# Kernel optimization log

Measured on AMD Instinct MI355X. Metric: run time of the kernel, lower is better.

## Reference

```python
import jax, jax.numpy as jnp
import numpy as np

B, N, NPOINT, K = 8, 8192, 1024, 32
MLP = [64, 64, 128]
EPS = 1e-5  # torch BatchNorm2d default eps


def setup_inputs() -> dict:
    key = jax.random.key(0)
    ks = jax.random.split(key, 1 + 2 * len(MLP))
    inp = {"xyz": jax.random.normal(ks[0], (B, N, 3), jnp.float32)}
    last = 3
    for i, o in enumerate(MLP):
        inp[f"w{i}"] = jax.random.normal(ks[1 + 2 * i], (o, last), jnp.float32) / np.float32(np.sqrt(last))
        inp[f"b{i}"] = jax.random.normal(ks[2 + 2 * i], (o,), jnp.float32) * 0.01
        inp[f"g{i}"] = jnp.ones((o,), jnp.float32)   # BN weight
        inp[f"be{i}"] = jnp.zeros((o,), jnp.float32)  # BN bias
        last = o
    return inp


def farthest_point_sample(xyz, npoint):
    # Sequential FPS; deterministic start at index 0 (original torch uses randint).
    Bb, Nn, _ = xyz.shape

    def step(carry, _):
        distance, farthest = carry
        centroid = jnp.take_along_axis(xyz, farthest[:, None, None], axis=1)  # [B,1,3]
        dist = jnp.sum((xyz - centroid) ** 2, -1)                              # [B,N]
        distance = jnp.minimum(distance, dist)
        nxt = jnp.argmax(distance, -1)
        return (distance, nxt), farthest

    init = (jnp.full((Bb, Nn), 1e10, xyz.dtype), jnp.zeros((Bb,), jnp.int32))
    _, cents = jax.lax.scan(step, init, None, length=npoint)
    return cents.T  # [B, npoint]


def _forward(xyz, params):
    fps_idx = farthest_point_sample(xyz, NPOINT)
    fps_idx = jax.lax.stop_gradient(fps_idx)
    new_xyz = jnp.take_along_axis(xyz, fps_idx[:, :, None], axis=1)  # [B,npoint,3]
    # squared pairwise distances [B, npoint, N]
    d = (jnp.sum(new_xyz ** 2, -1)[:, :, None]
         + jnp.sum(xyz ** 2, -1)[:, None, :]
         - 2.0 * jnp.einsum('bmc,bnc->bmn', new_xyz, xyz))
    _, idx = jax.lax.top_k(-d, K)  # k nearest neighbors, [B,npoint,k]
    grouped = jax.vmap(lambda pts, i: pts[i])(xyz, idx)  # [B,npoint,k,3]
    feat = grouped - new_xyz[:, :, None, :]              # grouped_xyz_norm
    # 1x1 Conv2d + BatchNorm2d(training stats) + ReLU stack
    for (w, b, g, be) in params:
        feat = jnp.einsum('bnkc,oc->bnko', feat, w) + b
        mu = jnp.mean(feat, axis=(0, 1, 2))
        var = jnp.var(feat, axis=(0, 1, 2))
        feat = g * (feat - mu) * jax.lax.rsqrt(var + EPS) + be
        feat = jax.nn.relu(feat)
    out = jnp.max(feat, axis=2)             # max over k neighbors -> [B,npoint,Cout]
    return new_xyz, jnp.transpose(out, (0, 2, 1))  # [B,npoint,3], [B,Cout,npoint]


def reference(xyz, w0, b0, g0, be0, w1, b1, g1, be1, w2, b2, g2, be2):
    params = [(w0, b0, g0, be0), (w1, b1, g1, be1), (w2, b2, g2, be2)]
    return _forward(xyz, params)
```

## Files before the change

### kernel.cpp

```cpp
#include <hip/hip_runtime.h>

#define NN_ 8192
#define MM_ 1024

#define DPP_UMAX64(K, CTRL)                                                     \
  {                                                                             \
    const int lo_ = (int)(unsigned int)(K);                                     \
    const int hi_ = (int)(unsigned int)((K) >> 32);                             \
    const int slo_ = __builtin_amdgcn_update_dpp(lo_, lo_, (CTRL), 0xf, 0xf, false); \
    const int shi_ = __builtin_amdgcn_update_dpp(hi_, hi_, (CTRL), 0xf, 0xf, false); \
    const unsigned long long ok_ =                                              \
        ((unsigned long long)(unsigned int)shi_ << 32) | (unsigned int)slo_;    \
    (K) = (ok_ > (K)) ? ok_ : (K);                                              \
  }

__global__ __launch_bounds__(256, 1) void fps_kernel(const float* __restrict__ xyz,
                                                     float* __restrict__ dout) {
  const int b = blockIdx.x;
  const int tid = threadIdx.x;
  const float* xb = xyz + (size_t)b * NN_ * 3;

  __shared__ float s_x[NN_], s_y[NN_], s_z[NN_];
  __shared__ float s_out[3 * MM_];
  __shared__ __align__(16) unsigned long long s_key[2][4];

  for (int i = tid; i < NN_; i += 256) {
    s_x[i] = xb[3 * i + 0];
    s_y[i] = xb[3 * i + 1];
    s_z[i] = xb[3 * i + 2];
  }
  __syncthreads();

  const int base = 32 * tid;
  float4 rx[8], ry[8], rz[8];
#pragma unroll
  for (int q = 0; q < 8; ++q) {
    rx[q] = *(const float4*)&s_x[base + 4 * q];
    ry[q] = *(const float4*)&s_y[base + 4 * q];
    rz[q] = *(const float4*)&s_z[base + 4 * q];
  }
  asm volatile("" ::: "memory");

  float pd[32];
#pragma unroll
  for (int j = 0; j < 32; ++j) pd[j] = 1e10f;

  const int lane = tid & 63;
  const int wv = tid >> 6;

  float cx = s_x[0], cy = s_y[0], cz = s_z[0];

  for (int it = 0; it < MM_; ++it) {
    if (tid == 0) {
      s_out[it * 3 + 0] = cx;
      s_out[it * 3 + 1] = cy;
      s_out[it * 3 + 2] = cz;
    }
    if (it == MM_ - 1) break;

    float ld = -1.0f;
    int lj = 0;
#define FPS_UPD(PX, PY, PZ, J)                                                 \
    {                                                                          \
      const float dx = __fsub_rn(PX, cx);                                      \
      const float dy = __fsub_rn(PY, cy);                                      \
      const float dz = __fsub_rn(PZ, cz);                                      \
      const float dist = __fadd_rn(                                            \
          __fadd_rn(__fmul_rn(dx, dx), __fmul_rn(dy, dy)), __fmul_rn(dz, dz)); \
      const float nd = fminf(pd[J], dist);                                     \
      pd[J] = nd;                                                              \
      if (nd > ld) { ld = nd; lj = (J); }                                      \
    }
#pragma unroll
    for (int q = 0; q < 8; ++q) {
      FPS_UPD(rx[q].x, ry[q].x, rz[q].x, 4 * q + 0)
      FPS_UPD(rx[q].y, ry[q].y, rz[q].y, 4 * q + 1)
      FPS_UPD(rx[q].z, ry[q].z, rz[q].z, 4 * q + 2)
      FPS_UPD(rx[q].w, ry[q].w, rz[q].w, 4 * q + 3)
    }
#undef FPS_UPD

    unsigned long long key =
        ((unsigned long long)__float_as_uint(ld) << 32) |
        (unsigned int)(8191 - (base + lj));
    DPP_UMAX64(key, 0x111)
    DPP_UMAX64(key, 0x112)
    DPP_UMAX64(key, 0x114)
    DPP_UMAX64(key, 0x118)
    DPP_UMAX64(key, 0x142)
    DPP_UMAX64(key, 0x143)
    if (lane == 63) s_key[it & 1][wv] = key;
    __syncthreads();

    const ulonglong2 ka = *(const ulonglong2*)&s_key[it & 1][0];
    const ulonglong2 kb = *(const ulonglong2*)&s_key[it & 1][2];
    unsigned long long best = (ka.x > ka.y) ? ka.x : ka.y;
    const unsigned long long bb = (kb.x > kb.y) ? kb.x : kb.y;
    best = (best > bb) ? best : bb;
    const int win = 8191 - (int)(unsigned int)(best & 0xFFFFFFFFu);
    cx = s_x[win];
    cy = s_y[win];
    cz = s_z[win];
  }

  __syncthreads();
  float* outx = dout + (size_t)b * MM_ * 3;
#pragma unroll
  for (int i = 0; i < 12; ++i) outx[i * 256 + tid] = s_out[i * 256 + tid];
}

__global__ __launch_bounds__(64) void knn_kernel(const float* __restrict__ xyz,
                                                 const float* __restrict__ dout,
                                                 int* __restrict__ knn) {
  __shared__ float dl[128][64];
  const int lane = threadIdx.x;
  const int center = blockIdx.x;
  const int b = center >> 10;
  const int m = center & 1023;
  const float* xb = xyz + (size_t)b * NN_ * 3;
  const float* cp = dout + (size_t)b * MM_ * 3 + m * 3;
  const float cx = cp[0], cy = cp[1], cz = cp[2];
  const float sm = __fadd_rn(__fadd_rn(__fmul_rn(cx, cx), __fmul_rn(cy, cy)),
                             __fmul_rn(cz, cz));

  float gd[16];
  int gj[16];
#pragma unroll
  for (int g = 0; g < 16; ++g) {
#pragma unroll
    for (int t = 0; t < 8; ++t) {
      const int jj = g * 8 + t;
      const int p = jj * 64 + lane;
      const float x = xb[p * 3 + 0];
      const float y = xb[p * 3 + 1];
      const float z = xb[p * 3 + 2];
      const float sn = __fadd_rn(__fadd_rn(__fmul_rn(x, x), __fmul_rn(y, y)),
                                 __fmul_rn(z, z));
      const float dt = __fmaf_rn(cz, z, __fmaf_rn(cy, y, __fmul_rn(cx, x)));
      const float d = __fsub_rn(__fadd_rn(sm, sn), __fmul_rn(2.0f, dt));
      dl[jj][lane] = d;
      if (t == 0) { gd[g] = d; gj[g] = jj; }
      else if (d < gd[g]) { gd[g] = d; gj[g] = jj; }
    }
  }

  int out_p = 0;
  const float INF = __int_as_float(0x7f800000);
  for (int r = 0; r < 32; ++r) {
    float ldv = gd[0];
    int ljj = gj[0];
#pragma unroll
    for (int g = 1; g < 16; ++g) {
      if (gd[g] < ldv) { ldv = gd[g]; ljj = gj[g]; }
    }
    int lp = ljj * 64 + lane;
#pragma unroll
    for (int mk = 1; mk < 64; mk <<= 1) {
      const float od = __shfl_xor(ldv, mk, 64);
      const int op = __shfl_xor(lp, mk, 64);
      const bool take = (od < ldv) || (od == ldv && op < lp);
      ldv = take ? od : ldv;
      lp = take ? op : lp;
    }
    if (lane == r) out_p = lp;
    const int wl = lp & 63;
    if (lane == wl) {
      const int jjs = lp >> 6;
      const int gs = jjs >> 3;
      dl[jjs][lane] = INF;
      float md = INF;
      int mj = 0;
#pragma unroll
      for (int t = 0; t < 8; ++t) {
        const int jj2 = gs * 8 + t;
        const float v = dl[jj2][lane];
        if (v < md) { md = v; mj = jj2; }
      }
#pragma unroll
      for (int g = 0; g < 16; ++g) {
        if (g == gs) { gd[g] = md; gj[g] = mj; }
      }
    }
  }
  if (lane < 32) knn[center * 32 + lane] = out_p;
}

__global__ void prep_kernel(const float* __restrict__ w1, const float* __restrict__ w2,
                            float* __restrict__ w1t, float* __restrict__ w2t) {
  const int t = blockIdx.x * 256 + threadIdx.x;
  if (t < 4096) { const int o = t >> 6, c = t & 63; w1t[c * 64 + o] = w1[t]; }
  if (t < 8192) { const int o = t >> 6, c = t & 63; w2t[c * 128 + o] = w2[t]; }
}

__global__ __launch_bounds__(256) void s1_kernel(const float* __restrict__ xyz,
                                                 const float* __restrict__ dout,
                                                 const int* __restrict__ knn,
                                                 const float* __restrict__ w0,
                                                 const float* __restrict__ b0,
                                                 float* __restrict__ part1) {
  const int tid = threadIdx.x;
  const int r = blockIdx.x * 256 + tid;
  const int cid = r >> 5;
  const int b = cid >> 10;
  const int m = cid & 1023;
  const int idx = knn[r];
  const float* pp = xyz + ((size_t)b * NN_ + idx) * 3;
  const float* cc = dout + ((size_t)b * MM_ + m) * 3;
  const float fx = pp[0] - cc[0];
  const float fy = pp[1] - cc[1];
  const float fz = pp[2] - cc[2];
  float acc[64];
#pragma unroll
  for (int o = 0; o < 64; ++o)
    acc[o] = fmaf(w0[o * 3 + 2], fz, fmaf(w0[o * 3 + 1], fy, fmaf(w0[o * 3 + 0], fx, b0[o])));
  const int lane = tid & 63;
  float* po = part1 + ((size_t)blockIdx.x * 4 + (tid >> 6)) * 128;
#pragma unroll
  for (int o = 0; o < 64; ++o) {
    float s = acc[o];
    float q = acc[o] * acc[o];
#pragma unroll
    for (int mk = 1; mk < 64; mk <<= 1) { s += __shfl_xor(s, mk, 64); q += __shfl_xor(q, mk, 64); }
    if (lane == 0) { po[o] = s; po[64 + o] = q; }
  }
}

__global__ __launch_bounds__(256) void rstat_kernel(const float* __restrict__ part, int C,
                                                    const float* __restrict__ g,
                                                    const float* __restrict__ be,
                                                    float* __restrict__ sc,
                                                    float* __restrict__ sh) {
  const int c = blockIdx.x;
  const int tid = threadIdx.x;
  float S = 0.0f, Q = 0.0f;
  for (int i = tid; i < 4096; i += 256) {
    S += part[(size_t)i * 2 * C + c];
    Q += part[(size_t)i * 2 * C + C + c];
  }
  const int lane = tid & 63;
#pragma unroll
  for (int mk = 1; mk < 64; mk <<= 1) { S += __shfl_xor(S, mk, 64); Q += __shfl_xor(Q, mk, 64); }
  __shared__ float rs[4], rq[4];
  if (lane == 0) { rs[tid >> 6] = S; rq[tid >> 6] = Q; }
  __syncthreads();
  if (tid == 0) {
    S = rs[0] + rs[1] + rs[2] + rs[3];
    Q = rq[0] + rq[1] + rq[2] + rq[3];
    const float mean = S * (1.0f / 262144.0f);
    const float var = fmaf(-mean, mean, Q * (1.0f / 262144.0f));
    const float s = g[c] * rsqrtf(var + 1e-5f);
    sc[c] = s;
    sh[c] = fmaf(-mean, s, be[c]);
  }
}

template <int STAGE>
__global__ __launch_bounds__(256) void chain_kernel(
    const float* __restrict__ xyz, const float* __restrict__ dout,
    const int* __restrict__ knn,
    const float* __restrict__ w0, const float* __restrict__ b0,
    const float* __restrict__ w1t, const float* __restrict__ b1,
    const float* __restrict__ w2t, const float* __restrict__ b2,
    const float* __restrict__ sc1, const float* __restrict__ sh1,
    const float* __restrict__ sc2, const float* __restrict__ sh2,
    const float* __restrict__ sc3, const float* __restrict__ sh3,
    float* __restrict__ part, float* __restrict__ outp) {
  __shared__ float f[64 * 256];
  const int tid = threadIdx.x;
  const int r = blockIdx.x * 256 + tid;
  const int cid = r >> 5;
  const int b = cid >> 10;
  const int m = cid & 1023;
  const int idx = knn[r];
  const float* pp = xyz + ((size_t)b * NN_ + idx) * 3;
  const float* cc = dout + ((size_t)b * MM_ + m) * 3;
  const float fx = pp[0] - cc[0];
  const float fy = pp[1] - cc[1];
  const float fz = pp[2] - cc[2];
  float acc[64];
#pragma unroll
  for (int o = 0; o < 64; ++o)
    acc[o] = fmaf(w0[o * 3 + 2], fz, fmaf(w0[o * 3 + 1], fy, fmaf(w0[o * 3 + 0], fx, b0[o])));
#pragma unroll
  for (int o = 0; o < 64; ++o)
    f[o * 256 + tid] = fmaxf(fmaf(acc[o], sc1[o], sh1[o]), 0.0f);
  float a2[64];
#pragma unroll
  for (int o = 0; o < 64; ++o) a2[o] = b1[o];
#pragma unroll 4
  for (int c = 0; c < 64; ++c) {
    const float x = f[c * 256 + tid];
#pragma unroll
    for (int o = 0; o < 64; ++o) a2[o] = fmaf(w1t[c * 64 + o], x, a2[o]);
  }
  const int lane = tid & 63;
  if constexpr (STAGE == 2) {
    float* po = part + ((size_t)blockIdx.x * 4 + (tid >> 6)) * 128;
#pragma unroll
    for (int o = 0; o < 64; ++o) {
      float s = a2[o], q = a2[o] * a2[o];
#pragma unroll
      for (int mk = 1; mk < 64; mk <<= 1) { s += __shfl_xor(s, mk, 64); q += __shfl_xor(q, mk, 64); }
      if (lane == 0) { po[o] = s; po[64 + o] = q; }
    }
    return;
  }
#pragma unroll
  for (int o = 0; o < 64; ++o)
    f[o * 256 + tid] = fmaxf(fmaf(a2[o], sc2[o], sh2[o]), 0.0f);
#pragma unroll
  for (int h = 0; h < 2; ++h) {
    float a3[64];
#pragma unroll
    for (int o = 0; o < 64; ++o) a3[o] = b2[h * 64 + o];
#pragma unroll 4
    for (int c = 0; c < 64; ++c) {
      const float x = f[c * 256 + tid];
#pragma unroll
      for (int o = 0; o < 64; ++o) a3[o] = fmaf(w2t[c * 128 + h * 64 + o], x, a3[o]);
    }
    if constexpr (STAGE == 3) {
      float* po = part + ((size_t)blockIdx.x * 4 + (tid >> 6)) * 256;
#pragma unroll
      for (int o = 0; o < 64; ++o) {
        float s = a3[o], q = a3[o] * a3[o];
#pragma unroll
        for (int mk = 1; mk < 64; mk <<= 1) { s += __shfl_xor(s, mk, 64); q += __shfl_xor(q, mk, 64); }
        if (lane == 0) { po[h * 64 + o] = s; po[128 + h * 64 + o] = q; }
      }
    } else {
#pragma unroll
      for (int o = 0; o < 64; ++o) {
        float v = fmaxf(fmaf(a3[o], sc3[h * 64 + o], sh3[h * 64 + o]), 0.0f);
#pragma unroll
        for (int mk = 1; mk < 32; mk <<= 1) v = fmaxf(v, __shfl_xor(v, mk, 64));
        if ((lane & 31) == 0)
          outp[24576 + (size_t)b * 131072 + (size_t)(h * 64 + o) * 1024 + m] = v;
      }
    }
  }
}

extern "C" void kernel_launch(void* const* d_in, const int* in_sizes, int n_in,
                              void* d_out, int out_size, void* d_ws, size_t ws_size,
                              hipStream_t stream) {
  const float* xyz = (const float*)d_in[0];
  const float* w0 = (const float*)d_in[1];
  const float* b0 = (const float*)d_in[2];
  const float* g0 = (const float*)d_in[3];
  const float* be0 = (const float*)d_in[4];
  const float* w1 = (const float*)d_in[5];
  const float* b1 = (const float*)d_in[6];
  const float* g1 = (const float*)d_in[7];
  const float* be1 = (const float*)d_in[8];
  const float* w2 = (const float*)d_in[9];
  const float* b2 = (const float*)d_in[10];
  const float* g2 = (const float*)d_in[11];
  const float* be2 = (const float*)d_in[12];
  float* out = (float*)d_out;
  char* ws = (char*)d_ws;

  int* knn = (int*)ws;
  float* part1 = (float*)(ws + (size_t)1 * (1 << 20));
  float* part2 = (float*)(ws + (size_t)3 * (1 << 20));
  float* part3 = (float*)(ws + (size_t)5 * (1 << 20));
  float* sc1 = (float*)(ws + (size_t)9 * (1 << 20));
  float* sh1 = sc1 + 64;
  float* sc2 = sh1 + 64;
  float* sh2 = sc2 + 64;
  float* sc3 = sh2 + 64;
  float* sh3 = sc3 + 128;
  float* w1t = sh3 + 128;
  float* w2t = w1t + 4096;

  fps_kernel<<<8, 256, 0, stream>>>(xyz, out);
  knn_kernel<<<8192, 64, 0, stream>>>(xyz, out, knn);
  prep_kernel<<<32, 256, 0, stream>>>(w1, w2, w1t, w2t);
  s1_kernel<<<1024, 256, 0, stream>>>(xyz, out, knn, w0, b0, part1);
  rstat_kernel<<<64, 256, 0, stream>>>(part1, 64, g0, be0, sc1, sh1);
  chain_kernel<2><<<1024, 256, 0, stream>>>(xyz, out, knn, w0, b0, w1t, b1, w2t, b2,
                                            sc1, sh1, sc2, sh2, sc3, sh3, part2, out);
  rstat_kernel<<<64, 256, 0, stream>>>(part2, 64, g1, be1, sc2, sh2);
  chain_kernel<3><<<1024, 256, 0, stream>>>(xyz, out, knn, w0, b0, w1t, b1, w2t, b2,
                                            sc1, sh1, sc2, sh2, sc3, sh3, part3, out);
  rstat_kernel<<<128, 256, 0, stream>>>(part3, 128, g2, be2, sc3, sh3);
  chain_kernel<4><<<1024, 256, 0, stream>>>(xyz, out, knn, w0, b0, w1t, b1, w2t, b2,
                                            sc1, sh1, sc2, sh2, sc3, sh3, part3, out);
}
```

Before: 1.722 ms.

## Pack FPS distance math, DPP kNN argmin, LDS-transpose BN statistics, fuse stage-3 halves

The FPS distance update now uses packed v_pk_add/v_pk_mul over pairs of points, roughly halving the VALU instruction count in the serial loop. The kNN wave argmin now reduces with 64-bit DPP keys (monotone float bits plus index) instead of two shuffles per xor step. Per-channel BN sum and sum-of-squares are computed by writing each wave's accumulators to LDS in skewed order and having each lane sum one channel, replacing 64 butterfly shuffle reductions per statistic. The stage-3 stats pass computes both 64-channel halves in one loop over inputs, which raises register pressure and adds a __syncthreads plus extra LDS use in s1.

```diff
diff --git a/kernel.cpp b/kernel.cpp
--- a/kernel.cpp
+++ b/kernel.cpp
@@ -2,6 +2,18 @@
 
 #define NN_ 8192
 #define MM_ 1024
+
+typedef float v2f __attribute__((ext_vector_type(2)));
+
+static __device__ __forceinline__ v2f pk_add(v2f a, v2f b) {
+  v2f d; asm("v_pk_add_f32 %0, %1, %2" : "=v"(d) : "v"(a), "v"(b)); return d;
+}
+static __device__ __forceinline__ v2f pk_sub(v2f a, v2f b) {
+  v2f d; asm("v_pk_add_f32 %0, %1, %2 neg_lo:[0,1] neg_hi:[0,1]" : "=v"(d) : "v"(a), "v"(b)); return d;
+}
+static __device__ __forceinline__ v2f pk_mul(v2f a, v2f b) {
+  v2f d; asm("v_pk_mul_f32 %0, %1, %2" : "=v"(d) : "v"(a), "v"(b)); return d;
+}
 
 #define DPP_UMAX64(K, CTRL)                                                     \
   {                                                                             \
@@ -13,6 +25,30 @@
         ((unsigned long long)(unsigned int)shi_ << 32) | (unsigned int)slo_;    \
     (K) = (ok_ > (K)) ? ok_ : (K);                                              \
   }
+#define DPP_UMIN64(K, CTRL)                                                     \
+  {                                                                             \
+    const int lo_ = (int)(unsigned int)(K);                                     \
+    const int hi_ = (int)(unsigned int)((K) >> 32);                             \
+    const int slo_ = __builtin_amdgcn_update_dpp(lo_, lo_, (CTRL), 0xf, 0xf, false); \
+    const int shi_ = __builtin_amdgcn_update_dpp(hi_, hi_, (CTRL), 0xf, 0xf, false); \
+    const unsigned long long ok_ =                                              \
+        ((unsigned long long)(unsigned int)shi_ << 32) | (unsigned int)slo_;    \
+    (K) = (ok_ < (K)) ? ok_ : (K);                                              \
+  }
+
+#define WAVE_STATS(T, ACC, PO_S, PO_Q)                                          \
+  {                                                                             \
+    _Pragma("unroll") for (int o_ = 0; o_ < 64; ++o_)                           \
+        (T)[o_ * 64 + ((lane + o_) & 63)] = (ACC)[o_];                          \
+    float s_ = 0.0f, q_ = 0.0f;                                                 \
+    _Pragma("unroll") for (int j_ = 0; j_ < 64; ++j_) {                         \
+      const float v_ = (T)[lane * 64 + ((j_ + lane) & 63)];                     \
+      s_ += v_;                                                                 \
+      q_ = fmaf(v_, v_, q_);                                                    \
+    }                                                                           \
+    (PO_S)[lane] = s_;                                                          \
+    (PO_Q)[lane] = q_;                                                          \
+  }
 
 __global__ __launch_bounds__(256, 1) void fps_kernel(const float* __restrict__ xyz,
                                                      float* __restrict__ dout) {
@@ -32,12 +68,18 @@
   __syncthreads();
 
   const int base = 32 * tid;
-  float4 rx[8], ry[8], rz[8];
+  v2f px2[16], py2[16], pz2[16];
 #pragma unroll
   for (int q = 0; q < 8; ++q) {
-    rx[q] = *(const float4*)&s_x[base + 4 * q];
-    ry[q] = *(const float4*)&s_y[base + 4 * q];
-    rz[q] = *(const float4*)&s_z[base + 4 * q];
+    const float4 xa = *(const float4*)&s_x[base + 4 * q];
+    const float4 ya = *(const float4*)&s_y[base + 4 * q];
+    const float4 za = *(const float4*)&s_z[base + 4 * q];
+    px2[2 * q] = (v2f){xa.x, xa.y};
+    px2[2 * q + 1] = (v2f){xa.z, xa.w};
+    py2[2 * q] = (v2f){ya.x, ya.y};
+    py2[2 * q + 1] = (v2f){ya.z, ya.w};
+    pz2[2 * q] = (v2f){za.x, za.y};
+    pz2[2 * q + 1] = (v2f){za.z, za.w};
   }
   asm volatile("" ::: "memory");
 
@@ -58,27 +100,24 @@
     }
     if (it == MM_ - 1) break;
 
+    const v2f c2x = (v2f){cx, cx};
+    const v2f c2y = (v2f){cy, cy};
+    const v2f c2z = (v2f){cz, cz};
     float ld = -1.0f;
     int lj = 0;
-#define FPS_UPD(PX, PY, PZ, J)                                                 \
-    {                                                                          \
-      const float dx = __fsub_rn(PX, cx);                                      \
-      const float dy = __fsub_rn(PY, cy);                                      \
-      const float dz = __fsub_rn(PZ, cz);                                      \
-      const float dist = __fadd_rn(                                            \
-          __fadd_rn(__fmul_rn(dx, dx), __fmul_rn(dy, dy)), __fmul_rn(dz, dz)); \
-      const float nd = fminf(pd[J], dist);                                     \
-      pd[J] = nd;                                                              \
-      if (nd > ld) { ld = nd; lj = (J); }                                      \
-    }
-#pragma unroll
-    for (int q = 0; q < 8; ++q) {
-      FPS_UPD(rx[q].x, ry[q].x, rz[q].x, 4 * q + 0)
-      FPS_UPD(rx[q].y, ry[q].y, rz[q].y, 4 * q + 1)
-      FPS_UPD(rx[q].z, ry[q].z, rz[q].z, 4 * q + 2)
-      FPS_UPD(rx[q].w, ry[q].w, rz[q].w, 4 * q + 3)
-    }
-#undef FPS_UPD
+#pragma unroll
+    for (int k = 0; k < 16; ++k) {
+      const v2f dx = pk_sub(px2[k], c2x);
+      const v2f dy = pk_sub(py2[k], c2y);
+      const v2f dz = pk_sub(pz2[k], c2z);
+      const v2f ss = pk_add(pk_add(pk_mul(dx, dx), pk_mul(dy, dy)), pk_mul(dz, dz));
+      const float nd0 = fminf(pd[2 * k], ss.x);
+      pd[2 * k] = nd0;
+      if (nd0 > ld) { ld = nd0; lj = 2 * k; }
+      const float nd1 = fminf(pd[2 * k + 1], ss.y);
+      pd[2 * k + 1] = nd1;
+      if (nd1 > ld) { ld = nd1; lj = 2 * k + 1; }
+    }
 
     unsigned long long key =
         ((unsigned long long)__float_as_uint(ld) << 32) |
@@ -153,15 +192,18 @@
     for (int g = 1; g < 16; ++g) {
       if (gd[g] < ldv) { ldv = gd[g]; ljj = gj[g]; }
     }
-    int lp = ljj * 64 + lane;
-#pragma unroll
-    for (int mk = 1; mk < 64; mk <<= 1) {
-      const float od = __shfl_xor(ldv, mk, 64);
-      const int op = __shfl_xor(lp, mk, 64);
-      const bool take = (od < ldv) || (od == ldv && op < lp);
-      ldv = take ? od : ldv;
-      lp = take ? op : lp;
-    }
+    const int lp0 = ljj * 64 + lane;
+    const unsigned db = __float_as_uint(ldv);
+    const unsigned mono = (db & 0x80000000u) ? ~db : (db | 0x80000000u);
+    unsigned long long kk =
+        ((unsigned long long)mono << 32) | (unsigned int)lp0;
+    DPP_UMIN64(kk, 0x111)
+    DPP_UMIN64(kk, 0x112)
+    DPP_UMIN64(kk, 0x114)
+    DPP_UMIN64(kk, 0x118)
+    DPP_UMIN64(kk, 0x142)
+    DPP_UMIN64(kk, 0x143)
+    const int lp = __builtin_amdgcn_readlane((int)(unsigned int)(kk & 0xFFFFFFFFull), 63);
     if (lane == r) out_p = lp;
     const int wl = lp & 63;
     if (lane == wl) {
@@ -198,6 +240,7 @@
                                                  const float* __restrict__ w0,
                                                  const float* __restrict__ b0,
                                                  float* __restrict__ part1) {
+  __shared__ float tw[4 * 4096];
   const int tid = threadIdx.x;
   const int r = blockIdx.x * 256 + tid;
   const int cid = r >> 5;
@@ -214,15 +257,10 @@
   for (int o = 0; o < 64; ++o)
     acc[o] = fmaf(w0[o * 3 + 2], fz, fmaf(w0[o * 3 + 1], fy, fmaf(w0[o * 3 + 0], fx, b0[o])));
   const int lane = tid & 63;
-  float* po = part1 + ((size_t)blockIdx.x * 4 + (tid >> 6)) * 128;
-#pragma unroll
-  for (int o = 0; o < 64; ++o) {
-    float s = acc[o];
-    float q = acc[o] * acc[o];
-#pragma unroll
-    for (int mk = 1; mk < 64; mk <<= 1) { s += __shfl_xor(s, mk, 64); q += __shfl_xor(q, mk, 64); }
-    if (lane == 0) { po[o] = s; po[64 + o] = q; }
-  }
+  const int wv = tid >> 6;
+  float* T = &tw[wv * 4096];
+  float* po = part1 + ((size_t)blockIdx.x * 4 + wv) * 128;
+  WAVE_STATS(T, acc, po, po + 64)
 }
 
 __global__ __launch_bounds__(256) void rstat_kernel(const float* __restrict__ part, int C,
@@ -277,6 +315,8 @@
   const float fx = pp[0] - cc[0];
   const float fy = pp[1] - cc[1];
   const float fz = pp[2] - cc[2];
+  const int lane = tid & 63;
+  const int wv = tid >> 6;
   float acc[64];
 #pragma unroll
   for (int o = 0; o < 64; ++o)
@@ -293,21 +333,35 @@
 #pragma unroll
     for (int o = 0; o < 64; ++o) a2[o] = fmaf(w1t[c * 64 + o], x, a2[o]);
   }
-  const int lane = tid & 63;
   if constexpr (STAGE == 2) {
-    float* po = part + ((size_t)blockIdx.x * 4 + (tid >> 6)) * 128;
-#pragma unroll
-    for (int o = 0; o < 64; ++o) {
-      float s = a2[o], q = a2[o] * a2[o];
-#pragma unroll
-      for (int mk = 1; mk < 64; mk <<= 1) { s += __shfl_xor(s, mk, 64); q += __shfl_xor(q, mk, 64); }
-      if (lane == 0) { po[o] = s; po[64 + o] = q; }
-    }
+    __syncthreads();
+    float* T = &f[wv * 4096];
+    float* po = part + ((size_t)blockIdx.x * 4 + wv) * 128;
+    WAVE_STATS(T, a2, po, po + 64)
     return;
   }
 #pragma unroll
   for (int o = 0; o < 64; ++o)
     f[o * 256 + tid] = fmaxf(fmaf(a2[o], sc2[o], sh2[o]), 0.0f);
+  if constexpr (STAGE == 3) {
+    float a3l[64], a3h[64];
+#pragma unroll
+    for (int o = 0; o < 64; ++o) { a3l[o] = b2[o]; a3h[o] = b2[64 + o]; }
+#pragma unroll 2
+    for (int c = 0; c < 64; ++c) {
+      const float x = f[c * 256 + tid];
+#pragma unroll
+      for (int o = 0; o < 64; ++o) a3l[o] = fmaf(w2t[c * 128 + o], x, a3l[o]);
+#pragma unroll
+      for (int o = 0; o < 64; ++o) a3h[o] = fmaf(w2t[c * 128 + 64 + o], x, a3h[o]);
+    }
+    __syncthreads();
+    float* T = &f[wv * 4096];
+    float* po = part + ((size_t)blockIdx.x * 4 + wv) * 256;
+    WAVE_STATS(T, a3l, po, po + 128)
+    WAVE_STATS(T, a3h, po + 64, po + 192)
+    return;
+  }
 #pragma unroll
   for (int h = 0; h < 2; ++h) {
     float a3[64];
@@ -319,24 +373,13 @@
 #pragma unroll
       for (int o = 0; o < 64; ++o) a3[o] = fmaf(w2t[c * 128 + h * 64 + o], x, a3[o]);
     }
-    if constexpr (STAGE == 3) {
-      float* po = part + ((size_t)blockIdx.x * 4 + (tid >> 6)) * 256;
-#pragma unroll
-      for (int o = 0; o < 64; ++o) {
-        float s = a3[o], q = a3[o] * a3[o];
-#pragma unroll
-        for (int mk = 1; mk < 64; mk <<= 1) { s += __shfl_xor(s, mk, 64); q += __shfl_xor(q, mk, 64); }
-        if (lane == 0) { po[h * 64 + o] = s; po[128 + h * 64 + o] = q; }
-      }
-    } else {
-#pragma unroll
-      for (int o = 0; o < 64; ++o) {
-        float v = fmaxf(fmaf(a3[o], sc3[h * 64 + o], sh3[h * 64 + o]), 0.0f);
-#pragma unroll
-        for (int mk = 1; mk < 32; mk <<= 1) v = fmaxf(v, __shfl_xor(v, mk, 64));
-        if ((lane & 31) == 0)
-          outp[24576 + (size_t)b * 131072 + (size_t)(h * 64 + o) * 1024 + m] = v;
-      }
+#pragma unroll
+    for (int o = 0; o < 64; ++o) {
+      float v = fmaxf(fmaf(a3[o], sc3[h * 64 + o], sh3[h * 64 + o]), 0.0f);
+#pragma unroll
+      for (int mk = 1; mk < 32; mk <<= 1) v = fmaxf(v, __shfl_xor(v, mk, 64));
+      if ((lane & 31) == 0)
+        outp[24576 + (size_t)b * 131072 + (size_t)(h * 64 + o) * 1024 + m] = v;
     }
   }
 }
```

Result: faster. 1.634 ms (-5.1%).
